# Kernel optimization log

Measured on AMD Instinct MI355X. Metric: run time of the kernel, lower is better.

The kernel has to match this reference:

```python
import jax, jax.numpy as jnp
import numpy as np

N = 100000   # nodes
E1 = 300000  # GINEConv (down) edges
E2 = 150000  # GraphConv (up) edges
D = 256      # hidden_dim
BN_EPS = 1e-5


def _bn_eval(h, gamma, beta, mean, var):
    # BatchNorm1d in eval mode (running stats)
    return (h - mean) * (gamma / jnp.sqrt(var + BN_EPS)) + beta


def setup_inputs() -> dict:
    key = jax.random.key(0)
    ks = jax.random.split(key, 12)
    s = 1.0 / np.sqrt(D)
    inp = {
        # forward args
        "x": jax.random.normal(ks[0], (N, D), dtype=jnp.float32),
        "edge_index": jax.random.randint(ks[1], (2, E1), 0, N, dtype=jnp.int64),
        "edge_attr_emb": jax.random.normal(ks[2], (E1, D), dtype=jnp.float32),
        "v_idx": jax.random.randint(ks[3], (2, E2), 0, N, dtype=jnp.int64),
        # GINEConv params
        "eps": jnp.zeros((), dtype=jnp.float32),  # train_eps, init 0
        "w1a": jax.random.normal(ks[4], (D, D), dtype=jnp.float32) * s,
        "b1a": jnp.zeros((D,), dtype=jnp.float32),
        "bn1_g": jnp.ones((D,), dtype=jnp.float32),
        "bn1_b": jnp.zeros((D,), dtype=jnp.float32),
        "bn1_m": jnp.zeros((D,), dtype=jnp.float32),
        "bn1_v": jnp.ones((D,), dtype=jnp.float32),
        "w1b": jax.random.normal(ks[5], (D, D), dtype=jnp.float32) * s,
        "b1b": jnp.zeros((D,), dtype=jnp.float32),
        # GraphConv params (lin_rel has bias, lin_root has no bias)
        "gc_w_rel": jax.random.normal(ks[6], (D, D), dtype=jnp.float32) * s,
        "gc_b_rel": jnp.zeros((D,), dtype=jnp.float32),
        "gc_w_root": jax.random.normal(ks[7], (D, D), dtype=jnp.float32) * s,
        # residual mixing + outer BN
        "alpha1": jnp.float32(0.5),
        "alpha2": jnp.float32(0.5),
        "bn_g": jnp.ones((D,), dtype=jnp.float32),
        "bn_b": jnp.zeros((D,), dtype=jnp.float32),
        "bn_m": jnp.zeros((D,), dtype=jnp.float32),
        "bn_v": jnp.ones((D,), dtype=jnp.float32),
    }
    return inp


def reference(x, edge_index, edge_attr_emb, v_idx, eps,
              w1a, b1a, bn1_g, bn1_b, bn1_m, bn1_v, w1b, b1b,
              gc_w_rel, gc_b_rel, gc_w_root,
              alpha1, alpha2, bn_g, bn_b, bn_m, bn_v):
    # ----- GINEConv: out = nn((1+eps)*x + sum_j relu(x_j + e_ji)) -----
    src, dst = edge_index[0], edge_index[1]
    msg = jax.nn.relu(x[src] + edge_attr_emb)                 # [E1, D] gather + add
    aggr = jax.ops.segment_sum(msg, dst, num_segments=N)      # scatter-add -> [N, D]
    h = (1.0 + eps) * x + aggr
    # nn1: Linear -> BN(eval) -> ReLU -> Dropout(eval=id) -> Linear
    h = jax.nn.relu(_bn_eval(h @ w1a.T + b1a, bn1_g, bn1_b, bn1_m, bn1_v))
    h_down = h @ w1b.T + b1b

    # ----- GraphConv (aggr='add'): lin_rel(sum_j x_j) + lin_root(x) -----
    src2, dst2 = v_idx[0], v_idx[1]
    aggr2 = jax.ops.segment_sum(x[src2], dst2, num_segments=N)  # [N, D]
    h_up = aggr2 @ gc_w_rel.T + gc_b_rel + x @ gc_w_root.T

    # ----- residual mix + BN + ReLU -----
    out = x + alpha1 * h_down + alpha2 * h_up
    return jax.nn.relu(_bn_eval(out, bn_g, bn_b, bn_m, bn_v))
```

## Files before the change

### kernel.cpp

```cpp
#include <hip/hip_runtime.h>
#include <hip/hip_bf16.h>

typedef __bf16 bf16_t;
typedef bf16_t bf16x8 __attribute__((ext_vector_type(8)));
typedef bf16_t bf16x4 __attribute__((ext_vector_type(4)));
typedef float  f32x4  __attribute__((ext_vector_type(4)));

#define NN 100000
#define E1N 300000
#define E2N 150000
#define DD 256
#define BNEPS 1e-5f
#define CAP1 32
#define CAP2 16

#define SWZ(row, col) ((col) ^ (((row) & 7) << 3))

__device__ __forceinline__ void glds16(const bf16_t* src, bf16_t* ldsbase) {
  __builtin_amdgcn_global_load_lds(
      (const __attribute__((address_space(1))) void*)src,
      (__attribute__((address_space(3))) void*)ldsbase, 16, 0, 0);
}

__global__ void prep_scalars(const float* b1a, const float* g1, const float* be1,
                             const float* m1, const float* v1,
                             const float* b1b, const float* gbrel,
                             const float* a1p, const float* a2p,
                             const float* g2, const float* be2,
                             const float* m2, const float* v2,
                             float* fold1, float* c2, float* s2f) {
  int c = threadIdx.x;
  float s1 = g1[c] * rsqrtf(v1[c] + BNEPS);
  fold1[c] = (b1a[c] - m1[c]) * s1 + be1[c];
  float s2 = g2[c] * rsqrtf(v2[c] + BNEPS);
  float cst = a1p[0] * b1b[c] + a2p[0] * gbrel[c];
  c2[c] = (cst - m2[c]) * s2 + be2[c];
  s2f[c] = s2;
}

__global__ void prep_w1(const float* w1a, const float* g1, const float* v1,
                        bf16_t* w1ab) {
  int o = blockIdx.x, i = threadIdx.x;
  float s1 = g1[o] * rsqrtf(v1[o] + BNEPS);
  w1ab[o * DD + i] = (bf16_t)(w1a[o * DD + i] * s1);
}

__global__ void prep_w2(const float* w1b, const float* wrel, const float* wroot,
                        const float* a1p, const float* a2p,
                        const float* g2, const float* v2, bf16_t* w2f) {
  int o = blockIdx.x, i = threadIdx.x;
  float s2 = g2[o] * rsqrtf(v2[o] + BNEPS);
  float a1 = a1p[0], a2 = a2p[0];
  w2f[o * 768 + i]       = (bf16_t)(w1b[o * DD + i]   * a1 * s2);
  w2f[o * 768 + 256 + i] = (bf16_t)(wrel[o * DD + i]  * a2 * s2);
  w2f[o * 768 + 512 + i] = (bf16_t)(wroot[o * DD + i] * a2 * s2);
}

__global__ void cast_x(const float* __restrict__ x, bf16_t* __restrict__ xbf,
                       int* __restrict__ cnt1, int* __restrict__ cnt2) {
  int gid = blockIdx.x * 256 + threadIdx.x;
  size_t i = (size_t)gid * 8;
  f32x4 v0 = *(const f32x4*)(x + i);
  f32x4 v1 = *(const f32x4*)(x + i + 4);
  bf16x8 o;
#pragma unroll
  for (int j = 0; j < 4; ++j) { o[j] = (bf16_t)v0[j]; o[4 + j] = (bf16_t)v1[j]; }
  *(bf16x8*)(xbf + i) = o;
  if (gid < NN) { cnt1[gid] = 0; cnt2[gid] = 0; }
}

__global__ void build_buckets(const int* __restrict__ ei, const int* __restrict__ vi,
                              int* cnt1, int* b1src, int* b1e,
                              int* cnt2, int* b2src) {
  int e = blockIdx.x * 256 + threadIdx.x;
  if (e < E1N) {
    int src = ei[e], dst = ei[E1N + e];
    int slot = atomicAdd(cnt1 + dst, 1);
    if (slot < CAP1) { b1src[dst * CAP1 + slot] = src; b1e[dst * CAP1 + slot] = e; }
  }
  if (e < E2N) {
    int src = vi[e], dst = vi[E2N + e];
    int slot = atomicAdd(cnt2 + dst, 1);
    if (slot < CAP2) b2src[dst * CAP2 + slot] = src;
  }
}

__global__ __launch_bounds__(256) void aggregate(
    const bf16_t* __restrict__ xbf, const float* epsp,
    const float* __restrict__ eattr,
    const int* __restrict__ cnt1, const int* __restrict__ b1src,
    const int* __restrict__ b1e,
    const int* __restrict__ cnt2, const int* __restrict__ b2src,
    bf16_t* __restrict__ aggr1_bf, bf16_t* __restrict__ aggr2_bf) {
  const int wid = threadIdx.x >> 6, lane = threadIdx.x & 63;
  const int col = lane * 4;
  const int nb = blockIdx.x * 3;

  if (wid < 3) {
    int n = nb + wid;
    if (n >= NN) return;
    float sc = 1.0f + epsp[0];
    bf16x4 xv = *(const bf16x4*)(xbf + (size_t)n * DD + col);
    f32x4 acc;
#pragma unroll
    for (int j = 0; j < 4; ++j) acc[j] = (float)xv[j] * sc;
    int cnt = cnt1[n]; cnt = cnt < CAP1 ? cnt : CAP1;
    const int* bs = b1src + n * CAP1;
    const int* be = b1e + n * CAP1;
    int i = 0;
    for (; i + 1 < cnt; i += 2) {
      int s0 = bs[i], e0 = be[i], s1 = bs[i + 1], e1 = be[i + 1];
      bf16x4 a0 = *(const bf16x4*)(xbf + (size_t)s0 * DD + col);
      f32x4  q0 = *(const f32x4*)(eattr + (size_t)e0 * DD + col);
      bf16x4 a1 = *(const bf16x4*)(xbf + (size_t)s1 * DD + col);
      f32x4  q1 = *(const f32x4*)(eattr + (size_t)e1 * DD + col);
#pragma unroll
      for (int j = 0; j < 4; ++j) {
        float m0 = (float)a0[j] + q0[j];
        float m1 = (float)a1[j] + q1[j];
        acc[j] += (m0 > 0.f ? m0 : 0.f) + (m1 > 0.f ? m1 : 0.f);
      }
    }
    if (i < cnt) {
      int s0 = bs[i], e0 = be[i];
      bf16x4 a0 = *(const bf16x4*)(xbf + (size_t)s0 * DD + col);
      f32x4  q0 = *(const f32x4*)(eattr + (size_t)e0 * DD + col);
#pragma unroll
      for (int j = 0; j < 4; ++j) {
        float m0 = (float)a0[j] + q0[j];
        acc[j] += (m0 > 0.f ? m0 : 0.f);
      }
    }
    bf16x4 o1;
#pragma unroll
    for (int j = 0; j < 4; ++j) o1[j] = (bf16_t)acc[j];
    *(bf16x4*)(aggr1_bf + (size_t)n * DD + col) = o1;
  } else {
    for (int k = 0; k < 3; ++k) {
      int n = nb + k;
      if (n >= NN) break;
      f32x4 acc = {0.f, 0.f, 0.f, 0.f};
      int cnt = cnt2[n]; cnt = cnt < CAP2 ? cnt : CAP2;
      const int* bs = b2src + n * CAP2;
      int i = 0;
      for (; i + 1 < cnt; i += 2) {
        int s0 = bs[i], s1 = bs[i + 1];
        bf16x4 a0 = *(const bf16x4*)(xbf + (size_t)s0 * DD + col);
        bf16x4 a1 = *(const bf16x4*)(xbf + (size_t)s1 * DD + col);
#pragma unroll
        for (int j = 0; j < 4; ++j) acc[j] += (float)a0[j] + (float)a1[j];
      }
      if (i < cnt) {
        int s0 = bs[i];
        bf16x4 a0 = *(const bf16x4*)(xbf + (size_t)s0 * DD + col);
#pragma unroll
        for (int j = 0; j < 4; ++j) acc[j] += (float)a0[j];
      }
      bf16x4 o2;
#pragma unroll
      for (int j = 0; j < 4; ++j) o2[j] = (bf16_t)acc[j];
      *(bf16x4*)(aggr2_bf + (size_t)n * DD + col) = o2;
    }
  }
}

__global__ __launch_bounds__(512) void gemm1(const bf16_t* __restrict__ aggr1_bf,
                                             const bf16_t* __restrict__ w1ab,
                                             const float* __restrict__ fold1,
                                             bf16_t* __restrict__ t1) {
  __shared__ bf16_t As[128][64];
  __shared__ bf16_t Bs[256][64];
  const int tid = threadIdx.x;
  const int m0 = blockIdx.x * 128;
  const int lane = tid & 63, wid = tid >> 6;
  const int wr = wid >> 2, wc = wid & 3;
  const int lr = lane & 15, kg = (lane >> 4) * 8;
  const int lrow = lane >> 3;
  const int lcol = ((lane & 7) ^ (lane >> 3)) * 8;

  f32x4 acc[4][4] = {};

  for (int kt = 0; kt < 4; ++kt) {
    const int k0 = kt * 64;
#pragma unroll
    for (int i = 0; i < 2; ++i) {
      int r0 = wid * 16 + i * 8;
      glds16(aggr1_bf + (size_t)(m0 + r0 + lrow) * DD + k0 + lcol, &As[r0][0]);
    }
#pragma unroll
    for (int i = 0; i < 4; ++i) {
      int r0 = wid * 32 + i * 8;
      glds16(w1ab + (size_t)(r0 + lrow) * DD + k0 + lcol, &Bs[r0][0]);
    }
    __syncthreads();
#pragma unroll
    for (int kk = 0; kk < 2; ++kk) {
      bf16x8 af[4], bfr[4];
#pragma unroll
      for (int m = 0; m < 4; ++m) {
        int r = wr * 64 + m * 16 + lr;
        af[m] = *(const bf16x8*)&As[r][SWZ(r, kk * 32 + kg)];
      }
#pragma unroll
      for (int n = 0; n < 4; ++n) {
        int r = wc * 64 + n * 16 + lr;
        bfr[n] = *(const bf16x8*)&Bs[r][SWZ(r, kk * 32 + kg)];
      }
#pragma unroll
      for (int m = 0; m < 4; ++m)
#pragma unroll
        for (int n = 0; n < 4; ++n)
          acc[m][n] = __builtin_amdgcn_mfma_f32_16x16x32_bf16(af[m], bfr[n], acc[m][n], 0, 0, 0);
    }
    __syncthreads();
  }

  const int rg = lane >> 4;
#pragma unroll
  for (int n = 0; n < 4; ++n) {
    int gc = wc * 64 + n * 16 + lr;
    float fo = fold1[gc];
#pragma unroll
    for (int m = 0; m < 4; ++m) {
      int gr0 = m0 + wr * 64 + m * 16 + rg * 4;
#pragma unroll
      for (int r = 0; r < 4; ++r) {
        int gr = gr0 + r;
        if (gr < NN) {
          float v = acc[m][n][r] + fo;
          t1[(size_t)gr * DD + gc] = (bf16_t)(v > 0.f ? v : 0.f);
        }
      }
    }
  }
}

__global__ __launch_bounds__(512) void gemm2(const bf16_t* __restrict__ t1,
                                             const bf16_t* __restrict__ aggr2_bf,
                                             const bf16_t* __restrict__ xbf,
                                             const bf16_t* __restrict__ w2f,
                                             const float* __restrict__ c2,
                                             const float* __restrict__ s2f,
                                             float* __restrict__ out) {
  __shared__ bf16_t As[128][64];
  __shared__ bf16_t Bs[256][64];
  const int tid = threadIdx.x;
  const int m0 = blockIdx.x * 128;
  const int lane = tid & 63, wid = tid >> 6;
  const int wr = wid >> 2, wc = wid & 3;
  const int lr = lane & 15, kg = (lane >> 4) * 8;
  const int lrow = lane >> 3;
  const int lcol = ((lane & 7) ^ (lane >> 3)) * 8;

  f32x4 acc[4][4] = {};

  for (int kt = 0; kt < 12; ++kt) {
    const bf16_t* Asrc = (kt < 4) ? t1 : (kt < 8 ? aggr2_bf : xbf);
    const int k0 = (kt & 3) * 64;
#pragma unroll
    for (int i = 0; i < 2; ++i) {
      int r0 = wid * 16 + i * 8;
      glds16(Asrc + (size_t)(m0 + r0 + lrow) * DD + k0 + lcol, &As[r0][0]);
    }
#pragma unroll
    for (int i = 0; i < 4; ++i) {
      int r0 = wid * 32 + i * 8;
      glds16(w2f + (size_t)(r0 + lrow) * 768 + kt * 64 + lcol, &Bs[r0][0]);
    }
    __syncthreads();
#pragma unroll
    for (int kk = 0; kk < 2; ++kk) {
      bf16x8 af[4], bfr[4];
#pragma unroll
      for (int m = 0; m < 4; ++m) {
        int r = wr * 64 + m * 16 + lr;
        af[m] = *(const bf16x8*)&As[r][SWZ(r, kk * 32 + kg)];
      }
#pragma unroll
      for (int n = 0; n < 4; ++n) {
        int r = wc * 64 + n * 16 + lr;
        bfr[n] = *(const bf16x8*)&Bs[r][SWZ(r, kk * 32 + kg)];
      }
#pragma unroll
      for (int m = 0; m < 4; ++m)
#pragma unroll
        for (int n = 0; n < 4; ++n)
          acc[m][n] = __builtin_amdgcn_mfma_f32_16x16x32_bf16(af[m], bfr[n], acc[m][n], 0, 0, 0);
    }
    __syncthreads();
  }

  const int rg = lane >> 4;
#pragma unroll
  for (int n = 0; n < 4; ++n) {
    int gc = wc * 64 + n * 16 + lr;
    float c2v = c2[gc];
    float s2v = s2f[gc];
#pragma unroll
    for (int m = 0; m < 4; ++m) {
      int gr0 = m0 + wr * 64 + m * 16 + rg * 4;
#pragma unroll
      for (int r = 0; r < 4; ++r) {
        int gr = gr0 + r;
        if (gr < NN) {
          float v = acc[m][n][r] + c2v + (float)xbf[(size_t)gr * DD + gc] * s2v;
          out[(size_t)gr * DD + gc] = (v > 0.f ? v : 0.f);
        }
      }
    }
  }
}

extern "C" void kernel_launch(void* const* d_in, const int* in_sizes, int n_in,
                              void* d_out, int out_size, void* d_ws, size_t ws_size,
                              hipStream_t stream) {
  const float* x     = (const float*)d_in[0];
  const int*   ei    = (const int*)d_in[1];
  const float* eattr = (const float*)d_in[2];
  const int*   vi    = (const int*)d_in[3];
  const float* epsp  = (const float*)d_in[4];
  const float* w1a   = (const float*)d_in[5];
  const float* b1a   = (const float*)d_in[6];
  const float* bn1g  = (const float*)d_in[7];
  const float* bn1b  = (const float*)d_in[8];
  const float* bn1m  = (const float*)d_in[9];
  const float* bn1v  = (const float*)d_in[10];
  const float* w1b   = (const float*)d_in[11];
  const float* b1b   = (const float*)d_in[12];
  const float* wrel  = (const float*)d_in[13];
  const float* gbrel = (const float*)d_in[14];
  const float* wroot = (const float*)d_in[15];
  const float* a1p   = (const float*)d_in[16];
  const float* a2p   = (const float*)d_in[17];
  const float* bng   = (const float*)d_in[18];
  const float* bnb   = (const float*)d_in[19];
  const float* bnm   = (const float*)d_in[20];
  const float* bnv   = (const float*)d_in[21];

  char* ws = (char*)d_ws;
  bf16_t* aggr1_bf = (bf16_t*)ws;
  bf16_t* aggr2_bf = (bf16_t*)(ws + 51200000);
  bf16_t* xbf      = (bf16_t*)(ws + 102400000);
  bf16_t* w1ab     = (bf16_t*)(ws + 153600000);
  bf16_t* w2f      = (bf16_t*)(ws + 153731072);
  float*  fold1    = (float*)(ws + 154124288);
  float*  c2       = (float*)(ws + 154125312);
  float*  s2f      = (float*)(ws + 154126336);
  int*    cnt1     = (int*)(ws + 154127360);
  int*    cnt2     = (int*)(ws + 154527360);
  int*    b1src    = (int*)(ws + 154927360);
  int*    b1e      = (int*)(ws + 167727360);
  int*    b2src    = (int*)(ws + 180527360);
  bf16_t* t1       = (bf16_t*)(ws + 186927360);

  prep_scalars<<<1, 256, 0, stream>>>(b1a, bn1g, bn1b, bn1m, bn1v, b1b, gbrel,
                                      a1p, a2p, bng, bnb, bnm, bnv, fold1, c2, s2f);
  prep_w1<<<256, 256, 0, stream>>>(w1a, bn1g, bn1v, w1ab);
  prep_w2<<<256, 256, 0, stream>>>(w1b, wrel, wroot, a1p, a2p, bng, bnv, w2f);
  cast_x<<<12500, 256, 0, stream>>>(x, xbf, cnt1, cnt2);
  build_buckets<<<1172, 256, 0, stream>>>(ei, vi, cnt1, b1src, b1e, cnt2, b2src);
  aggregate<<<33334, 256, 0, stream>>>(xbf, epsp, eattr,
                                       cnt1, b1src, b1e, cnt2, b2src,
                                       aggr1_bf, aggr2_bf);
  gemm1<<<782, 512, 0, stream>>>(aggr1_bf, w1ab, fold1, t1);
  gemm2<<<782, 512, 0, stream>>>(t1, aggr2_bf, xbf, w2f, c2, s2f, (float*)d_out);
}
```

Before: 331.8 us.

## Fuse x cast into aggregate, split GEMM N-tiles and double-buffer LDS

Removes the separate cast_x kernel: the aggregate kernel now gathers fp32 x directly and writes the bf16 copy of x as a side output, and the counters are zeroed with a memset. Both GEMMs change from 512-thread 128x256 tiles to 256-thread 128x128 tiles over a 2D grid, with double-buffered LDS so the next K-slice loads while the current one is computed. The aim is to drop one full pass over x and hide global-to-LDS latency. The cost is that the gathers now read fp32 rows, twice the bytes per neighbour, and each A tile is loaded by two blocks.

```diff
diff --git a/kernel.cpp b/kernel.cpp
--- a/kernel.cpp
+++ b/kernel.cpp
@@ -56,19 +56,6 @@
   w2f[o * 768 + 512 + i] = (bf16_t)(wroot[o * DD + i] * a2 * s2);
 }
 
-__global__ void cast_x(const float* __restrict__ x, bf16_t* __restrict__ xbf,
-                       int* __restrict__ cnt1, int* __restrict__ cnt2) {
-  int gid = blockIdx.x * 256 + threadIdx.x;
-  size_t i = (size_t)gid * 8;
-  f32x4 v0 = *(const f32x4*)(x + i);
-  f32x4 v1 = *(const f32x4*)(x + i + 4);
-  bf16x8 o;
-#pragma unroll
-  for (int j = 0; j < 4; ++j) { o[j] = (bf16_t)v0[j]; o[4 + j] = (bf16_t)v1[j]; }
-  *(bf16x8*)(xbf + i) = o;
-  if (gid < NN) { cnt1[gid] = 0; cnt2[gid] = 0; }
-}
-
 __global__ void build_buckets(const int* __restrict__ ei, const int* __restrict__ vi,
                               int* cnt1, int* b1src, int* b1e,
                               int* cnt2, int* b2src) {
@@ -86,12 +73,13 @@
 }
 
 __global__ __launch_bounds__(256) void aggregate(
-    const bf16_t* __restrict__ xbf, const float* epsp,
+    const float* __restrict__ x, const float* epsp,
     const float* __restrict__ eattr,
     const int* __restrict__ cnt1, const int* __restrict__ b1src,
     const int* __restrict__ b1e,
     const int* __restrict__ cnt2, const int* __restrict__ b2src,
-    bf16_t* __restrict__ aggr1_bf, bf16_t* __restrict__ aggr2_bf) {
+    bf16_t* __restrict__ aggr1_bf, bf16_t* __restrict__ aggr2_bf,
+    bf16_t* __restrict__ xbf) {
   const int wid = threadIdx.x >> 6, lane = threadIdx.x & 63;
   const int col = lane * 4;
   const int nb = blockIdx.x * 3;
@@ -100,41 +88,42 @@
     int n = nb + wid;
     if (n >= NN) return;
     float sc = 1.0f + epsp[0];
-    bf16x4 xv = *(const bf16x4*)(xbf + (size_t)n * DD + col);
+    f32x4 xv = *(const f32x4*)(x + (size_t)n * DD + col);
     f32x4 acc;
 #pragma unroll
-    for (int j = 0; j < 4; ++j) acc[j] = (float)xv[j] * sc;
+    for (int j = 0; j < 4; ++j) acc[j] = xv[j] * sc;
     int cnt = cnt1[n]; cnt = cnt < CAP1 ? cnt : CAP1;
     const int* bs = b1src + n * CAP1;
     const int* be = b1e + n * CAP1;
     int i = 0;
     for (; i + 1 < cnt; i += 2) {
       int s0 = bs[i], e0 = be[i], s1 = bs[i + 1], e1 = be[i + 1];
-      bf16x4 a0 = *(const bf16x4*)(xbf + (size_t)s0 * DD + col);
-      f32x4  q0 = *(const f32x4*)(eattr + (size_t)e0 * DD + col);
-      bf16x4 a1 = *(const bf16x4*)(xbf + (size_t)s1 * DD + col);
-      f32x4  q1 = *(const f32x4*)(eattr + (size_t)e1 * DD + col);
+      f32x4 a0 = *(const f32x4*)(x + (size_t)s0 * DD + col);
+      f32x4 q0 = *(const f32x4*)(eattr + (size_t)e0 * DD + col);
+      f32x4 a1 = *(const f32x4*)(x + (size_t)s1 * DD + col);
+      f32x4 q1 = *(const f32x4*)(eattr + (size_t)e1 * DD + col);
 #pragma unroll
       for (int j = 0; j < 4; ++j) {
-        float m0 = (float)a0[j] + q0[j];
-        float m1 = (float)a1[j] + q1[j];
+        float m0 = a0[j] + q0[j];
+        float m1 = a1[j] + q1[j];
         acc[j] += (m0 > 0.f ? m0 : 0.f) + (m1 > 0.f ? m1 : 0.f);
       }
     }
     if (i < cnt) {
       int s0 = bs[i], e0 = be[i];
-      bf16x4 a0 = *(const bf16x4*)(xbf + (size_t)s0 * DD + col);
-      f32x4  q0 = *(const f32x4*)(eattr + (size_t)e0 * DD + col);
+      f32x4 a0 = *(const f32x4*)(x + (size_t)s0 * DD + col);
+      f32x4 q0 = *(const f32x4*)(eattr + (size_t)e0 * DD + col);
 #pragma unroll
       for (int j = 0; j < 4; ++j) {
-        float m0 = (float)a0[j] + q0[j];
+        float m0 = a0[j] + q0[j];
         acc[j] += (m0 > 0.f ? m0 : 0.f);
       }
     }
-    bf16x4 o1;
-#pragma unroll
-    for (int j = 0; j < 4; ++j) o1[j] = (bf16_t)acc[j];
+    bf16x4 o1, ox;
+#pragma unroll
+    for (int j = 0; j < 4; ++j) { o1[j] = (bf16_t)acc[j]; ox[j] = (bf16_t)xv[j]; }
     *(bf16x4*)(aggr1_bf + (size_t)n * DD + col) = o1;
+    *(bf16x4*)(xbf + (size_t)n * DD + col) = ox;
   } else {
     for (int k = 0; k < 3; ++k) {
       int n = nb + k;
@@ -145,16 +134,16 @@
       int i = 0;
       for (; i + 1 < cnt; i += 2) {
         int s0 = bs[i], s1 = bs[i + 1];
-        bf16x4 a0 = *(const bf16x4*)(xbf + (size_t)s0 * DD + col);
-        bf16x4 a1 = *(const bf16x4*)(xbf + (size_t)s1 * DD + col);
-#pragma unroll
-        for (int j = 0; j < 4; ++j) acc[j] += (float)a0[j] + (float)a1[j];
+        f32x4 a0 = *(const f32x4*)(x + (size_t)s0 * DD + col);
+        f32x4 a1 = *(const f32x4*)(x + (size_t)s1 * DD + col);
+#pragma unroll
+        for (int j = 0; j < 4; ++j) acc[j] += a0[j] + a1[j];
       }
       if (i < cnt) {
         int s0 = bs[i];
-        bf16x4 a0 = *(const bf16x4*)(xbf + (size_t)s0 * DD + col);
-#pragma unroll
-        for (int j = 0; j < 4; ++j) acc[j] += (float)a0[j];
+        f32x4 a0 = *(const f32x4*)(x + (size_t)s0 * DD + col);
+#pragma unroll
+        for (int j = 0; j < 4; ++j) acc[j] += a0[j];
       }
       bf16x4 o2;
 #pragma unroll
@@ -164,47 +153,50 @@
   }
 }
 
-__global__ __launch_bounds__(512) void gemm1(const bf16_t* __restrict__ aggr1_bf,
+__global__ __launch_bounds__(256) void gemm1(const bf16_t* __restrict__ aggr1_bf,
                                              const bf16_t* __restrict__ w1ab,
                                              const float* __restrict__ fold1,
                                              bf16_t* __restrict__ t1) {
-  __shared__ bf16_t As[128][64];
-  __shared__ bf16_t Bs[256][64];
+  __shared__ bf16_t As[2][128][64];
+  __shared__ bf16_t Bs[2][128][64];
   const int tid = threadIdx.x;
   const int m0 = blockIdx.x * 128;
+  const int n0 = blockIdx.y * 128;
   const int lane = tid & 63, wid = tid >> 6;
-  const int wr = wid >> 2, wc = wid & 3;
+  const int wr = wid >> 1, wc = wid & 1;
   const int lr = lane & 15, kg = (lane >> 4) * 8;
   const int lrow = lane >> 3;
   const int lcol = ((lane & 7) ^ (lane >> 3)) * 8;
 
   f32x4 acc[4][4] = {};
 
-  for (int kt = 0; kt < 4; ++kt) {
+  auto stage = [&](int b, int kt) {
     const int k0 = kt * 64;
-#pragma unroll
-    for (int i = 0; i < 2; ++i) {
-      int r0 = wid * 16 + i * 8;
-      glds16(aggr1_bf + (size_t)(m0 + r0 + lrow) * DD + k0 + lcol, &As[r0][0]);
-    }
 #pragma unroll
     for (int i = 0; i < 4; ++i) {
       int r0 = wid * 32 + i * 8;
-      glds16(w1ab + (size_t)(r0 + lrow) * DD + k0 + lcol, &Bs[r0][0]);
-    }
-    __syncthreads();
+      glds16(aggr1_bf + (size_t)(m0 + r0 + lrow) * DD + k0 + lcol, &As[b][r0][0]);
+      glds16(w1ab + (size_t)(n0 + r0 + lrow) * DD + k0 + lcol, &Bs[b][r0][0]);
+    }
+  };
+
+  stage(0, 0);
+  __syncthreads();
+  int cur = 0;
+  for (int kt = 0; kt < 4; ++kt) {
+    if (kt < 3) stage(cur ^ 1, kt + 1);
 #pragma unroll
     for (int kk = 0; kk < 2; ++kk) {
       bf16x8 af[4], bfr[4];
 #pragma unroll
       for (int m = 0; m < 4; ++m) {
         int r = wr * 64 + m * 16 + lr;
-        af[m] = *(const bf16x8*)&As[r][SWZ(r, kk * 32 + kg)];
+        af[m] = *(const bf16x8*)&As[cur][r][SWZ(r, kk * 32 + kg)];
       }
 #pragma unroll
       for (int n = 0; n < 4; ++n) {
         int r = wc * 64 + n * 16 + lr;
-        bfr[n] = *(const bf16x8*)&Bs[r][SWZ(r, kk * 32 + kg)];
+        bfr[n] = *(const bf16x8*)&Bs[cur][r][SWZ(r, kk * 32 + kg)];
       }
 #pragma unroll
       for (int m = 0; m < 4; ++m)
@@ -213,12 +205,13 @@
           acc[m][n] = __builtin_amdgcn_mfma_f32_16x16x32_bf16(af[m], bfr[n], acc[m][n], 0, 0, 0);
     }
     __syncthreads();
+    cur ^= 1;
   }
 
   const int rg = lane >> 4;
 #pragma unroll
   for (int n = 0; n < 4; ++n) {
-    int gc = wc * 64 + n * 16 + lr;
+    int gc = n0 + wc * 64 + n * 16 + lr;
     float fo = fold1[gc];
 #pragma unroll
     for (int m = 0; m < 4; ++m) {
@@ -235,51 +228,54 @@
   }
 }
 
-__global__ __launch_bounds__(512) void gemm2(const bf16_t* __restrict__ t1,
+__global__ __launch_bounds__(256) void gemm2(const bf16_t* __restrict__ t1,
                                              const bf16_t* __restrict__ aggr2_bf,
                                              const bf16_t* __restrict__ xbf,
                                              const bf16_t* __restrict__ w2f,
                                              const float* __restrict__ c2,
                                              const float* __restrict__ s2f,
                                              float* __restrict__ out) {
-  __shared__ bf16_t As[128][64];
-  __shared__ bf16_t Bs[256][64];
+  __shared__ bf16_t As[2][128][64];
+  __shared__ bf16_t Bs[2][128][64];
   const int tid = threadIdx.x;
   const int m0 = blockIdx.x * 128;
+  const int n0 = blockIdx.y * 128;
   const int lane = tid & 63, wid = tid >> 6;
-  const int wr = wid >> 2, wc = wid & 3;
+  const int wr = wid >> 1, wc = wid & 1;
   const int lr = lane & 15, kg = (lane >> 4) * 8;
   const int lrow = lane >> 3;
   const int lcol = ((lane & 7) ^ (lane >> 3)) * 8;
 
   f32x4 acc[4][4] = {};
 
-  for (int kt = 0; kt < 12; ++kt) {
+  auto stage = [&](int b, int kt) {
     const bf16_t* Asrc = (kt < 4) ? t1 : (kt < 8 ? aggr2_bf : xbf);
     const int k0 = (kt & 3) * 64;
 #pragma unroll
-    for (int i = 0; i < 2; ++i) {
-      int r0 = wid * 16 + i * 8;
-      glds16(Asrc + (size_t)(m0 + r0 + lrow) * DD + k0 + lcol, &As[r0][0]);
-    }
-#pragma unroll
     for (int i = 0; i < 4; ++i) {
       int r0 = wid * 32 + i * 8;
-      glds16(w2f + (size_t)(r0 + lrow) * 768 + kt * 64 + lcol, &Bs[r0][0]);
-    }
-    __syncthreads();
+      glds16(Asrc + (size_t)(m0 + r0 + lrow) * DD + k0 + lcol, &As[b][r0][0]);
+      glds16(w2f + (size_t)(n0 + r0 + lrow) * 768 + kt * 64 + lcol, &Bs[b][r0][0]);
+    }
+  };
+
+  stage(0, 0);
+  __syncthreads();
+  int cur = 0;
+  for (int kt = 0; kt < 12; ++kt) {
+    if (kt < 11) stage(cur ^ 1, kt + 1);
 #pragma unroll
     for (int kk = 0; kk < 2; ++kk) {
       bf16x8 af[4], bfr[4];
 #pragma unroll
       for (int m = 0; m < 4; ++m) {
         int r = wr * 64 + m * 16 + lr;
-        af[m] = *(const bf16x8*)&As[r][SWZ(r, kk * 32 + kg)];
+        af[m] = *(const bf16x8*)&As[cur][r][SWZ(r, kk * 32 + kg)];
       }
 #pragma unroll
       for (int n = 0; n < 4; ++n) {
         int r = wc * 64 + n * 16 + lr;
-        bfr[n] = *(const bf16x8*)&Bs[r][SWZ(r, kk * 32 + kg)];
+        bfr[n] = *(const bf16x8*)&Bs[cur][r][SWZ(r, kk * 32 + kg)];
       }
 #pragma unroll
       for (int m = 0; m < 4; ++m)
@@ -288,12 +284,13 @@
           acc[m][n] = __builtin_amdgcn_mfma_f32_16x16x32_bf16(af[m], bfr[n], acc[m][n], 0, 0, 0);
     }
     __syncthreads();
+    cur ^= 1;
   }
 
   const int rg = lane >> 4;
 #pragma unroll
   for (int n = 0; n < 4; ++n) {
-    int gc = wc * 64 + n * 16 + lr;
+    int gc = n0 + wc * 64 + n * 16 + lr;
     float c2v = c2[gc];
     float s2v = s2f[gc];
 #pragma unroll
@@ -357,11 +354,12 @@
                                       a1p, a2p, bng, bnb, bnm, bnv, fold1, c2, s2f);
   prep_w1<<<256, 256, 0, stream>>>(w1a, bn1g, bn1v, w1ab);
   prep_w2<<<256, 256, 0, stream>>>(w1b, wrel, wroot, a1p, a2p, bng, bnv, w2f);
-  cast_x<<<12500, 256, 0, stream>>>(x, xbf, cnt1, cnt2);
+  hipMemsetAsync(cnt1, 0, 800000, stream);
   build_buckets<<<1172, 256, 0, stream>>>(ei, vi, cnt1, b1src, b1e, cnt2, b2src);
-  aggregate<<<33334, 256, 0, stream>>>(xbf, epsp, eattr,
+  aggregate<<<33334, 256, 0, stream>>>(x, epsp, eattr,
                                        cnt1, b1src, b1e, cnt2, b2src,
-                                       aggr1_bf, aggr2_bf);
-  gemm1<<<782, 512, 0, stream>>>(aggr1_bf, w1ab, fold1, t1);
-  gemm2<<<782, 512, 0, stream>>>(t1, aggr2_bf, xbf, w2f, c2, s2f, (float*)d_out);
-}
+                                       aggr1_bf, aggr2_bf, xbf);
+  gemm1<<<dim3(782, 2), 256, 0, stream>>>(aggr1_bf, w1ab, fold1, t1);
+  gemm2<<<dim3(782, 2), 256, 0, stream>>>(t1, aggr2_bf, xbf, w2f, c2, s2f,
+                                          (float*)d_out);
+}
```

Result: slower. 397.4 us (+19.8%).
